# Optimization experiments

Measured on AMD Instinct MI355X. Metric: run time of the kernel, lower is better.

## Reference

```python
import jax, jax.numpy as jnp
import numpy as np
import math
from jax import lax

DIM = 96
D_MODEL = 2 * DIM            # SS2D d_model
D_INNER = 2 * D_MODEL        # expand = 2
D_STATE = 16
DT_RANK = math.ceil(D_MODEL / 16)
K = 4
B_, H_, W_ = 2, 48, 48


def setup_inputs() -> dict:
    key = jax.random.key(0)
    ks = jax.random.split(key, 12)
    r = lambda k, s, sc=0.02: jax.random.normal(k, s, jnp.float32) * sc
    A = np.tile(np.arange(1, D_STATE + 1, dtype=np.float32)[None, :], (K * D_INNER, 1))
    return dict(
        x=jax.random.normal(ks[0], (B_, DIM, H_, W_), jnp.float32),
        w_init=r(ks[1], (D_MODEL, DIM)),
        b_init=r(ks[2], (D_MODEL,)),
        w_fina=r(ks[3], (DIM, D_MODEL)),
        b_fina=r(ks[4], (DIM,)),
        in_proj_w=r(ks[5], (2 * D_INNER, D_MODEL)),
        conv_w=r(ks[6], (D_INNER, 1, 3, 3), 0.1),
        conv_b=r(ks[7], (D_INNER,)),
        x_proj_w=r(ks[8], (K, DT_RANK + 2 * D_STATE, D_INNER)),
        dt_w=r(ks[9], (K, D_INNER, DT_RANK), 0.1),
        dt_b=r(ks[10], (K, D_INNER), 0.1),
        A_logs=jnp.asarray(np.log(A)),
        Ds=jnp.ones((K * D_INNER,), jnp.float32),
        ln_g=jnp.ones((D_INNER,), jnp.float32),
        ln_b=jnp.zeros((D_INNER,), jnp.float32),
        out_proj_w=r(ks[11], (D_MODEL, D_INNER)),
    )


def _gelu(x):
    return jax.nn.gelu(x, approximate=False)


def _conv1x1(x, w, b):
    # x: (b,c,h,w), w: (o,c)
    return jnp.einsum('oc,bchw->bohw', w, x) + b[None, :, None, None]


def _ss2d(x, in_proj_w, conv_w, conv_b, x_proj_w, dt_w, dt_b, A_logs, Ds, ln_g, ln_b, out_proj_w):
    # x: (b, h, w, d_model)
    b, h, w, _ = x.shape
    L = h * w
    xz = jnp.einsum('bhwc,oc->bhwo', x, in_proj_w)          # (b,h,w,2*d_inner)
    xx, z = jnp.split(xz, 2, axis=-1)
    xc = xx.transpose(0, 3, 1, 2)                            # (b, d_inner, h, w)
    xc = lax.conv_general_dilated(xc, conv_w, (1, 1), 'SAME',
                                  feature_group_count=D_INNER,
                                  dimension_numbers=('NCHW', 'OIHW', 'NCHW'))
    xc = jax.nn.silu(xc + conv_b[None, :, None, None])
    # 4 scan directions: hw, wh, reversed hw, reversed wh
    x_hw = xc.reshape(b, D_INNER, L)
    x_wh = xc.transpose(0, 1, 3, 2).reshape(b, D_INNER, L)
    xs = jnp.stack([x_hw, x_wh, x_hw[..., ::-1], x_wh[..., ::-1]], axis=1)   # (b,K,d,L)
    x_dbl = jnp.einsum('bkdl,kcd->bkcl', xs, x_proj_w)
    dts = x_dbl[:, :, :DT_RANK]                               # (b,K,r,L)
    Bs = x_dbl[:, :, DT_RANK:DT_RANK + D_STATE]               # (b,K,n,L)
    Cs = x_dbl[:, :, DT_RANK + D_STATE:]                      # (b,K,n,L)
    dts = jnp.einsum('bkrl,kdr->bkdl', dts, dt_w)
    delta = jax.nn.softplus(dts + dt_b[None, :, :, None])     # (b,K,d,L)
    A = -jnp.exp(A_logs).reshape(K, D_INNER, D_STATE)         # (K,d,n)
    Dm = Ds.reshape(K, D_INNER)
    # selective scan over L (time-major stacked inputs)
    u_t = xs.transpose(3, 0, 1, 2)      # (L,b,K,d)
    dt_t = delta.transpose(3, 0, 1, 2)  # (L,b,K,d)
    B_t = Bs.transpose(3, 0, 1, 2)      # (L,b,K,n)
    C_t = Cs.transpose(3, 0, 1, 2)      # (L,b,K,n)
    h0 = jnp.zeros((b, K, D_INNER, D_STATE), xs.dtype)

    def step(hst, inp):
        u, dt, Bv, Cv = inp
        dA = jnp.exp(dt[..., None] * A)                       # (b,K,d,n)
        hst = dA * hst + (dt * u)[..., None] * Bv[:, :, None, :]
        y = jnp.einsum('bkdn,bkn->bkd', hst, Cv)
        return hst, y

    _, ys = lax.scan(step, h0, (u_t, dt_t, B_t, C_t))         # (L,b,K,d)
    ys = ys.transpose(1, 2, 3, 0) + Dm[None, :, :, None] * xs  # (b,K,d,L)
    y1 = ys[:, 0]
    y3 = ys[:, 2][..., ::-1]
    y2 = ys[:, 1].reshape(b, D_INNER, w, h).transpose(0, 1, 3, 2).reshape(b, D_INNER, L)
    y4 = ys[:, 3][..., ::-1].reshape(b, D_INNER, w, h).transpose(0, 1, 3, 2).reshape(b, D_INNER, L)
    y = (y1 + y2 + y3 + y4).transpose(0, 2, 1).reshape(b, h, w, D_INNER)
    mu = y.mean(-1, keepdims=True)
    var = y.var(-1, keepdims=True)
    y = (y - mu) / jnp.sqrt(var + 1e-5) * ln_g + ln_b
    y = y * jax.nn.silu(z)
    return jnp.einsum('bhwd,od->bhwo', y, out_proj_w)         # (b,h,w,d_model)


def _forward(x, w_init, b_init, w_fina, b_fina, in_proj_w, conv_w, conv_b,
             x_proj_w, dt_w, dt_b, A_logs, Ds, ln_g, ln_b, out_proj_w):
    x1 = _gelu(_conv1x1(x, w_init, b_init))                   # (b,2*dim,h,w)
    x0 = x1
    xt = x1.transpose(0, 2, 3, 1)                             # b h w c
    y = _ss2d(xt, in_proj_w, conv_w, conv_b, x_proj_w, dt_w, dt_b,
              A_logs, Ds, ln_g, ln_b, out_proj_w)
    y = y.transpose(0, 3, 1, 2)
    return _gelu(_conv1x1(y + x0, w_fina, b_fina))            # (b,dim,h,w)


def reference(x, w_init, b_init, w_fina, b_fina, in_proj_w, conv_w, conv_b,
              x_proj_w, dt_w, dt_b, A_logs, Ds, ln_g, ln_b, out_proj_w):
    return _forward(x, w_init, b_init, w_fina, b_fina, in_proj_w, conv_w, conv_b,
                    x_proj_w, dt_w, dt_b, A_logs, Ds, ln_g, ln_b, out_proj_w)
```

## Files before the change

kernel.cpp:

```cpp
#include <hip/hip_runtime.h>
#include <math.h>

#define LL 2304
#define HH 48
#define WW 48
#define BB 2
#define CI 96
#define DM 192
#define DI 384
#define KK 4
#define RR 12
#define NN 16
#define KC 44
#define CH 96
#define LEN 24

__device__ __forceinline__ float gelu_f(float x){
    return 0.5f*x*(1.0f+erff(x*0.70710678118654752f));
}
__device__ __forceinline__ float silu_f(float x){
    return x/(1.0f+__expf(-x));
}
__device__ __forceinline__ float softplus_f(float x){
    return fmaxf(x,0.0f) + log1pf(__expf(-fabsf(x)));
}

template<int C, int OT>
__device__ __forceinline__ void gemmN_acc(const float* __restrict__ xb, const float* __restrict__ w,
        int o0, float* wl, float acc[OT], int tid){
    for(int idx=tid; idx<OT*C; idx+=256) wl[idx] = w[(size_t)o0*C + idx];
    __syncthreads();
    #pragma unroll 2
    for(int c=0;c<C;c+=4){
        float x0=xb[(size_t)(c+0)*LL], x1=xb[(size_t)(c+1)*LL];
        float x2=xb[(size_t)(c+2)*LL], x3=xb[(size_t)(c+3)*LL];
        #pragma unroll
        for(int o=0;o<OT;o++){
            float4 wq = *reinterpret_cast<const float4*>(wl + o*C + c);
            acc[o] = fmaf(wq.x,x0, fmaf(wq.y,x1, fmaf(wq.z,x2, fmaf(wq.w,x3, acc[o]))));
        }
    }
}

__global__ __launch_bounds__(256) void k_init(const float* __restrict__ x, const float* __restrict__ w,
        const float* __restrict__ bias, float* __restrict__ x1){
    __shared__ float wl[8*CI];
    int l = blockIdx.x*256 + threadIdx.x;
    int o0 = blockIdx.y*8; int b = blockIdx.z;
    float acc[8];
    #pragma unroll
    for(int j=0;j<8;j++) acc[j] = bias[o0+j];
    gemmN_acc<CI,8>(x + (size_t)b*CI*LL + l, w, o0, wl, acc, threadIdx.x);
    float* ob = x1 + (size_t)b*DM*LL + o0*LL + l;
    #pragma unroll
    for(int j=0;j<8;j++) ob[j*LL] = gelu_f(acc[j]);
}

__global__ __launch_bounds__(256) void k_inproj(const float* __restrict__ x1, const float* __restrict__ w,
        float* __restrict__ xx, float* __restrict__ z){
    __shared__ float wl[16*DM];
    int l = blockIdx.x*256 + threadIdx.x;
    int o0 = blockIdx.y*16; int b = blockIdx.z;
    float acc[16];
    #pragma unroll
    for(int j=0;j<16;j++) acc[j] = 0.f;
    gemmN_acc<DM,16>(x1 + (size_t)b*DM*LL + l, w, o0, wl, acc, threadIdx.x);
    float* ob = (o0 < DI) ? (xx + (size_t)b*DI*LL + o0*LL + l)
                          : (z  + (size_t)b*DI*LL + (o0-DI)*LL + l);
    #pragma unroll
    for(int j=0;j<16;j++) ob[j*LL] = acc[j];
}

__global__ __launch_bounds__(256) void k_dwconv(const float* __restrict__ xx, const float* __restrict__ cw,
        const float* __restrict__ cb, float* __restrict__ xc){
    int l = blockIdx.x*256 + threadIdx.x;
    int d = blockIdx.y; int b = blockIdx.z;
    int h = l/WW, w = l%WW;
    const float* src = xx + ((size_t)b*DI + d)*LL;
    float acc = cb[d];
    #pragma unroll
    for(int dh=-1;dh<=1;dh++){
        int hh = h+dh; if(hh<0||hh>=HH) continue;
        #pragma unroll
        for(int dw=-1;dw<=1;dw++){
            int w2 = w+dw; if(w2<0||w2>=WW) continue;
            acc += cw[d*9 + (dh+1)*3 + (dw+1)] * src[hh*WW + w2];
        }
    }
    xc[((size_t)b*DI + d)*LL + l] = silu_f(acc);
}

__global__ __launch_bounds__(256) void k_proj(const float* __restrict__ xc, const float* __restrict__ w,
        float* __restrict__ pj){
    __shared__ float wl[8*DI];
    int l = blockIdx.x*256 + threadIdx.x;
    int o0 = blockIdx.y*8; int b = blockIdx.z;
    float acc[8];
    #pragma unroll
    for(int j=0;j<8;j++) acc[j] = 0.f;
    gemmN_acc<DI,8>(xc + (size_t)b*DI*LL + l, w, o0, wl, acc, threadIdx.x);
    float* ob = pj + ((size_t)b*(KK*KC) + o0)*LL + l;
    #pragma unroll
    for(int j=0;j<8;j++) ob[j*LL] = acc[j];
}

__global__ __launch_bounds__(256) void k_transpose(const float* __restrict__ xc, const float* __restrict__ z,
        float* __restrict__ xcT, float* __restrict__ zT){
    __shared__ float tile[32][33];
    int which = blockIdx.z >> 1;
    int b = blockIdx.z & 1;
    const float* src = which ? z : xc;
    float* dst = which ? zT : xcT;
    int l0 = blockIdx.x*32, d0 = blockIdx.y*32;
    int tx = threadIdx.x & 31, ty = threadIdx.x >> 5;
    #pragma unroll
    for(int j=0;j<4;j++)
        tile[ty+8*j][tx] = src[((size_t)b*DI + d0+ty+8*j)*LL + l0+tx];
    __syncthreads();
    #pragma unroll
    for(int j=0;j<4;j++)
        dst[((size_t)b*LL + l0+ty+8*j)*DI + d0+tx] = tile[tx][ty+8*j];
}

__global__ __launch_bounds__(256) void k_delta(const float* __restrict__ pj, const float* __restrict__ dtw,
        const float* __restrict__ dtb, float* __restrict__ deltaT){
    __shared__ float pjs[RR*32];
    int p0 = blockIdx.x*32;
    int bk = blockIdx.z; int b = bk>>2, k = bk&3;
    int lane = threadIdx.x & 63, sub = threadIdx.x >> 6;
    int d = blockIdx.y*64 + lane;
    const float* pjb = pj + ((size_t)b*(KK*KC) + k*KC)*LL;
    for(int idx=threadIdx.x; idx<RR*32; idx+=256){
        int r = idx>>5, pp = idx&31;
        pjs[idx] = pjb[(size_t)r*LL + p0+pp];
    }
    __syncthreads();
    float wr[RR];
    #pragma unroll
    for(int r=0;r<RR;r++) wr[r] = dtw[((size_t)k*DI + d)*RR + r];
    float dtbv = dtb[k*DI + d];
    #pragma unroll
    for(int i=0;i<8;i++){
        int pp = sub*8+i;
        float acc = dtbv;
        #pragma unroll
        for(int r=0;r<RR;r++) acc += wr[r]*pjs[r*32+pp];
        deltaT[((size_t)bk*LL + p0+pp)*DI + d] = softplus_f(acc);
    }
}

__device__ __forceinline__ int perm_pos(int k, int l){
    int lk = (k>=2) ? (LL-1-l) : l;
    return (k&1) ? ((lk%WW)*WW + lk/WW) : lk;
}

__global__ __launch_bounds__(384) void k_scan1(const float* __restrict__ xcT, const float* __restrict__ pj,
        const float* __restrict__ deltaT, const float* __restrict__ alogs,
        float* __restrict__ gbuf, float* __restrict__ Sbuf){
    __shared__ float bs[LEN*16];
    int chunk = blockIdx.x;
    int bk = blockIdx.y; int b = bk>>2, k = bk&3;
    int lane = threadIdx.x & 63, wv = threadIdx.x >> 6;
    int d = wv*64 + lane;
    const float* pjb = pj + ((size_t)b*(KK*KC) + k*KC)*LL;
    for(int idx=threadIdx.x; idx<LEN*16; idx+=384){
        int s = idx>>4, n = idx&15;
        int p = perm_pos(k, chunk*LEN+s);
        bs[idx] = pjb[(size_t)(RR+n)*LL + p];
    }
    __syncthreads();
    float a[NN], h[NN];
    #pragma unroll
    for(int n=0;n<NN;n++){ a[n] = -__expf(alogs[((size_t)k*DI + d)*NN + n]); h[n]=0.f; }
    float S = 0.f;
    const float* dptr = deltaT + (size_t)bk*LL*DI + d;
    const float* uptr = xcT + (size_t)b*LL*DI + d;
    for(int s=0;s<LEN;s++){
        int p = perm_pos(k, chunk*LEN+s);
        float dt = dptr[(size_t)p*DI];
        float u  = uptr[(size_t)p*DI];
        S += dt;
        float du = dt*u;
        #pragma unroll
        for(int nq=0;nq<4;nq++){
            float4 Bq = *reinterpret_cast<const float4*>(bs + s*16 + nq*4);
            h[nq*4+0] = __expf(dt*a[nq*4+0])*h[nq*4+0] + du*Bq.x;
            h[nq*4+1] = __expf(dt*a[nq*4+1])*h[nq*4+1] + du*Bq.y;
            h[nq*4+2] = __expf(dt*a[nq*4+2])*h[nq*4+2] + du*Bq.z;
            h[nq*4+3] = __expf(dt*a[nq*4+3])*h[nq*4+3] + du*Bq.w;
        }
    }
    int base = (bk*CH + chunk)*NN;
    #pragma unroll
    for(int n=0;n<NN;n++) gbuf[(size_t)(base+n)*DI + d] = h[n];
    Sbuf[(size_t)(bk*CH + chunk)*DI + d] = S;
}

__global__ __launch_bounds__(256) void k_scan2(const float* __restrict__ alogs, const float* __restrict__ Sbuf,
        float* __restrict__ gbuf){
    int id = blockIdx.x*256 + threadIdx.x;
    int d = id % DI;
    int n = (id/DI) % NN;
    int bk = id/(DI*NN);
    int k = bk & 3;
    float a = -__expf(alogs[((size_t)k*DI + d)*NN + n]);
    float h = 0.f;
    for(int j=0;j<CH;j++){
        float S = Sbuf[(size_t)(bk*CH + j)*DI + d];
        size_t gi = (size_t)((bk*CH + j)*NN + n)*DI + d;
        float g = gbuf[gi];
        gbuf[gi] = h;
        h = __expf(a*S)*h + g;
    }
}

__global__ __launch_bounds__(384) void k_scan3(const float* __restrict__ xcT, const float* __restrict__ pj,
        const float* deltaT, const float* __restrict__ alogs,
        const float* __restrict__ gbuf, float* yout){
    __shared__ float bs[LEN*32];
    int chunk = blockIdx.x;
    int bk = blockIdx.y; int b = bk>>2, k = bk&3;
    int lane = threadIdx.x & 63, wv = threadIdx.x >> 6;
    int d = wv*64 + lane;
    const float* pjb = pj + ((size_t)b*(KK*KC) + k*KC)*LL;
    for(int idx=threadIdx.x; idx<LEN*32; idx+=384){
        int s = idx>>5, c = idx&31;
        int p = perm_pos(k, chunk*LEN+s);
        bs[idx] = pjb[(size_t)(RR+c)*LL + p];
    }
    __syncthreads();
    float a[NN], h[NN];
    int base = (bk*CH + chunk)*NN;
    #pragma unroll
    for(int n=0;n<NN;n++){
        a[n] = -__expf(alogs[((size_t)k*DI + d)*NN + n]);
        h[n] = gbuf[(size_t)(base+n)*DI + d];
    }
    const float* dptr = deltaT + (size_t)bk*LL*DI + d;
    const float* uptr = xcT + (size_t)b*LL*DI + d;
    float* yptr = yout + (size_t)bk*LL*DI + d;
    for(int s=0;s<LEN;s++){
        int p = perm_pos(k, chunk*LEN+s);
        float dt = dptr[(size_t)p*DI];
        float u  = uptr[(size_t)p*DI];
        float du = dt*u;
        float y = 0.f;
        #pragma unroll
        for(int nq=0;nq<4;nq++){
            float4 Bq = *reinterpret_cast<const float4*>(bs + s*32 + nq*4);
            float4 Cq = *reinterpret_cast<const float4*>(bs + s*32 + 16 + nq*4);
            h[nq*4+0] = __expf(dt*a[nq*4+0])*h[nq*4+0] + du*Bq.x;  y += h[nq*4+0]*Cq.x;
            h[nq*4+1] = __expf(dt*a[nq*4+1])*h[nq*4+1] + du*Bq.y;  y += h[nq*4+1]*Cq.y;
            h[nq*4+2] = __expf(dt*a[nq*4+2])*h[nq*4+2] + du*Bq.z;  y += h[nq*4+2]*Cq.z;
            h[nq*4+3] = __expf(dt*a[nq*4+3])*h[nq*4+3] + du*Bq.w;  y += h[nq*4+3]*Cq.w;
        }
        yptr[(size_t)p*DI] = y;
    }
}

__global__ __launch_bounds__(256) void k_merge(const float* __restrict__ yout, const float* __restrict__ xcT,
        const float* __restrict__ zT, const float* __restrict__ Ds,
        const float* __restrict__ lng, const float* __restrict__ lnb,
        float* __restrict__ ygT){
    __shared__ float tile[32*385];
    int p0 = blockIdx.x*32; int b = blockIdx.y;
    for(int idx=threadIdx.x; idx<32*DI; idx+=256){
        int pp = idx/DI, d = idx%DI; int p = p0+pp;
        float dsum = Ds[d] + Ds[DI+d] + Ds[2*DI+d] + Ds[3*DI+d];
        float v = dsum * xcT[((size_t)b*LL + p)*DI + d];
        #pragma unroll
        for(int kk=0;kk<4;kk++) v += yout[((size_t)(b*4+kk)*LL + p)*DI + d];
        tile[pp*385 + d] = v;
    }
    __syncthreads();
    int lane = threadIdx.x & 63, wv = threadIdx.x >> 6;
    for(int i=0;i<8;i++){
        int pp = wv*8 + i; int p = p0+pp;
        float s1=0.f, s2=0.f;
        float vals[6];
        #pragma unroll
        for(int j=0;j<6;j++){ float v = tile[pp*385 + lane + 64*j]; vals[j]=v; s1+=v; s2+=v*v; }
        #pragma unroll
        for(int m=1;m<64;m<<=1){ s1 += __shfl_xor(s1,m); s2 += __shfl_xor(s2,m); }
        float mu = s1*(1.0f/DI);
        float var = s2*(1.0f/DI) - mu*mu;
        float rstd = rsqrtf(var + 1e-5f);
        #pragma unroll
        for(int j=0;j<6;j++){
            int c = lane + 64*j;
            float zv = zT[((size_t)b*LL + p)*DI + c];
            float y = (vals[j]-mu)*rstd*lng[c] + lnb[c];
            tile[pp*385 + c] = y * silu_f(zv);
        }
    }
    __syncthreads();
    for(int idx=threadIdx.x; idx<32*DI; idx+=256){
        int pp = idx & 31, d = idx >> 5;
        ygT[((size_t)b*DI + d)*LL + p0 + pp] = tile[pp*385 + d];
    }
}

__global__ __launch_bounds__(256) void k_outproj(const float* __restrict__ ygT, const float* __restrict__ w,
        const float* __restrict__ x1, float* __restrict__ yo){
    __shared__ float wl[8*DI];
    int l = blockIdx.x*256 + threadIdx.x;
    int o0 = blockIdx.y*8; int b = blockIdx.z;
    float acc[8];
    #pragma unroll
    for(int j=0;j<8;j++) acc[j] = 0.f;
    gemmN_acc<DI,8>(ygT + (size_t)b*DI*LL + l, w, o0, wl, acc, threadIdx.x);
    const float* rb = x1 + (size_t)b*DM*LL + o0*LL + l;
    float* ob = yo + (size_t)b*DM*LL + o0*LL + l;
    #pragma unroll
    for(int j=0;j<8;j++) ob[j*LL] = acc[j] + rb[j*LL];
}

__global__ __launch_bounds__(256) void k_final(const float* __restrict__ yo,
        const float* __restrict__ w, const float* __restrict__ bias, float* __restrict__ out){
    __shared__ float wl[4*DM];
    int l = blockIdx.x*256 + threadIdx.x;
    int o0 = blockIdx.y*4; int b = blockIdx.z;
    float acc[4];
    #pragma unroll
    for(int j=0;j<4;j++) acc[j] = bias[o0+j];
    gemmN_acc<DM,4>(yo + (size_t)b*DM*LL + l, w, o0, wl, acc, threadIdx.x);
    float* ob = out + (size_t)b*CI*LL + o0*LL + l;
    #pragma unroll
    for(int j=0;j<4;j++) ob[j*LL] = gelu_f(acc[j]);
}

extern "C" void kernel_launch(void* const* d_in, const int* in_sizes, int n_in,
                              void* d_out, int out_size, void* d_ws, size_t ws_size,
                              hipStream_t stream) {
    const float* x        = (const float*)d_in[0];
    const float* w_init   = (const float*)d_in[1];
    const float* b_init   = (const float*)d_in[2];
    const float* w_fina   = (const float*)d_in[3];
    const float* b_fina   = (const float*)d_in[4];
    const float* in_proj_w= (const float*)d_in[5];
    const float* conv_w   = (const float*)d_in[6];
    const float* conv_b   = (const float*)d_in[7];
    const float* x_proj_w = (const float*)d_in[8];
    const float* dt_w     = (const float*)d_in[9];
    const float* dt_b     = (const float*)d_in[10];
    const float* A_logs   = (const float*)d_in[11];
    const float* Ds       = (const float*)d_in[12];
    const float* ln_g     = (const float*)d_in[13];
    const float* ln_b     = (const float*)d_in[14];
    const float* out_proj_w=(const float*)d_in[15];

    float* ws = (float*)d_ws;
    float* x1   = ws;
    float* xx   = x1 + 884736;
    float* z    = xx + 1769472;
    float* xc   = z  + 1769472;
    float* xcT  = xc + 1769472;
    float* zT   = xcT+ 1769472;
    float* pj   = zT + 1769472;
    float* deltaT = pj + 811008;

    float* gbuf = xx;
    float* Sbuf = xx + 4718592;
    float* yout = deltaT;
    float* ygT  = xx;
    float* yo   = z;

    dim3 blk(256);
    k_init   <<<dim3(9,24,BB), blk, 0, stream>>>(x, w_init, b_init, x1);
    k_inproj <<<dim3(9,48,BB), blk, 0, stream>>>(x1, in_proj_w, xx, z);
    k_dwconv <<<dim3(9,DI,BB), blk, 0, stream>>>(xx, conv_w, conv_b, xc);
    k_proj   <<<dim3(9,22,BB), blk, 0, stream>>>(xc, x_proj_w, pj);
    k_transpose<<<dim3(72,12,2*BB), blk, 0, stream>>>(xc, z, xcT, zT);
    k_delta  <<<dim3(72,6,BB*KK), blk, 0, stream>>>(pj, dt_w, dt_b, deltaT);
    k_scan1  <<<dim3(CH,BB*KK), dim3(384), 0, stream>>>(xcT, pj, deltaT, A_logs, gbuf, Sbuf);
    k_scan2  <<<dim3(192), blk, 0, stream>>>(A_logs, Sbuf, gbuf);
    k_scan3  <<<dim3(CH,BB*KK), dim3(384), 0, stream>>>(xcT, pj, deltaT, A_logs, gbuf, yout);
    k_merge  <<<dim3(72,BB), blk, 0, stream>>>(yout, xcT, zT, Ds, ln_g, ln_b, ygT);
    k_outproj<<<dim3(9,24,BB), blk, 0, stream>>>(ygT, out_proj_w, x1, yo);
    k_final  <<<dim3(9,24,BB), blk, 0, stream>>>(yo, w_fina, b_fina, (float*)d_out);
}
```

Before: 360.7 us.

## Move in/x/out projection GEMMs to split-bf16 MFMA with transposed activations

Replaces the scalar FP32 GEMMs for in_proj, x_proj and out_proj with MFMA 16x16x32 bf16 kernels. Each operand is split into high and low bf16 parts, and three products are summed to keep near-FP32 accuracy. Producer kernels (init, transpose, merge) now also emit token-major bf16 hi/lo copies, and a new kernel converts the weights on every call. The aim is to cut ALU-bound GEMM time. In exchange it adds extra buffer writes, per-call weight conversion, and direct global loads without LDS staging, and it drops the low*low term.

```diff
diff --git a/kernel.cpp b/kernel.cpp
--- a/kernel.cpp
+++ b/kernel.cpp
@@ -15,6 +15,9 @@
 #define CH 96
 #define LEN 24
 
+typedef short bf16x8 __attribute__((ext_vector_type(8)));
+typedef float f32x4 __attribute__((ext_vector_type(4)));
+
 __device__ __forceinline__ float gelu_f(float x){
     return 0.5f*x*(1.0f+erff(x*0.70710678118654752f));
 }
@@ -23,6 +26,16 @@
 }
 __device__ __forceinline__ float softplus_f(float x){
     return fmaxf(x,0.0f) + log1pf(__expf(-fabsf(x)));
+}
+__device__ __forceinline__ unsigned short bf16_rne(float x){
+    unsigned u = __float_as_uint(x);
+    unsigned r = (u + 0x7FFFu + ((u>>16)&1u)) >> 16;
+    return (unsigned short)r;
+}
+__device__ __forceinline__ void split_bf16(float x, unsigned short& h, unsigned short& l){
+    h = bf16_rne(x);
+    float fh = __uint_as_float(((unsigned)h)<<16);
+    l = bf16_rne(x - fh);
 }
 
 template<int C, int OT>
@@ -42,8 +55,56 @@
     }
 }
 
+__global__ __launch_bounds__(256) void k_convw(const float* __restrict__ ipw, const float* __restrict__ xpw,
+        const float* __restrict__ opw, short* __restrict__ wh_ip, short* __restrict__ wl_ip,
+        short* __restrict__ wh_xp, short* __restrict__ wl_xp,
+        short* __restrict__ wh_op, short* __restrict__ wl_op){
+    int idx = blockIdx.x*256 + threadIdx.x;
+    unsigned short h, l;
+    if(idx < 147456){
+        split_bf16(ipw[idx], h, l); wh_ip[idx]=h; wl_ip[idx]=l;
+    } else if(idx < 147456+67584){
+        int j = idx - 147456;
+        split_bf16(xpw[j], h, l); wh_xp[j]=h; wl_xp[j]=l;
+    } else {
+        int j = idx - 215040;
+        split_bf16(opw[j], h, l); wh_op[j]=h; wl_op[j]=l;
+    }
+}
+
+template<int K>
+__device__ __forceinline__ void mfma_core(const short* __restrict__ Ah, const short* __restrict__ Al,
+        const short* __restrict__ Bh, const short* __restrict__ Bl, f32x4 acc[2][4]){
+    int lane = threadIdx.x & 63;
+    int rl = lane & 15, g = lane >> 4;
+    #pragma unroll
+    for(int kc=0; kc<K; kc+=32){
+        bf16x8 ah[2], al[2], bh[4], bl[4];
+        #pragma unroll
+        for(int mi=0;mi<2;mi++){
+            ah[mi] = *reinterpret_cast<const bf16x8*>(Ah + (size_t)(mi*16+rl)*K + kc + g*8);
+            al[mi] = *reinterpret_cast<const bf16x8*>(Al + (size_t)(mi*16+rl)*K + kc + g*8);
+        }
+        #pragma unroll
+        for(int ni=0;ni<4;ni++){
+            bh[ni] = *reinterpret_cast<const bf16x8*>(Bh + (size_t)(ni*16+rl)*K + kc + g*8);
+            bl[ni] = *reinterpret_cast<const bf16x8*>(Bl + (size_t)(ni*16+rl)*K + kc + g*8);
+        }
+        #pragma unroll
+        for(int mi=0;mi<2;mi++){
+            #pragma unroll
+            for(int ni=0;ni<4;ni++){
+                acc[mi][ni] = __builtin_amdgcn_mfma_f32_16x16x32_bf16(ah[mi], bh[ni], acc[mi][ni], 0,0,0);
+                acc[mi][ni] = __builtin_amdgcn_mfma_f32_16x16x32_bf16(ah[mi], bl[ni], acc[mi][ni], 0,0,0);
+                acc[mi][ni] = __builtin_amdgcn_mfma_f32_16x16x32_bf16(al[mi], bh[ni], acc[mi][ni], 0,0,0);
+            }
+        }
+    }
+}
+
 __global__ __launch_bounds__(256) void k_init(const float* __restrict__ x, const float* __restrict__ w,
-        const float* __restrict__ bias, float* __restrict__ x1){
+        const float* __restrict__ bias, float* __restrict__ x1,
+        short* __restrict__ x1Th, short* __restrict__ x1Tl){
     __shared__ float wl[8*CI];
     int l = blockIdx.x*256 + threadIdx.x;
     int o0 = blockIdx.y*8; int b = blockIdx.z;
@@ -52,23 +113,51 @@
     for(int j=0;j<8;j++) acc[j] = bias[o0+j];
     gemmN_acc<CI,8>(x + (size_t)b*CI*LL + l, w, o0, wl, acc, threadIdx.x);
     float* ob = x1 + (size_t)b*DM*LL + o0*LL + l;
-    #pragma unroll
-    for(int j=0;j<8;j++) ob[j*LL] = gelu_f(acc[j]);
-}
-
-__global__ __launch_bounds__(256) void k_inproj(const float* __restrict__ x1, const float* __restrict__ w,
+    unsigned hw[4], lw[4];
+    #pragma unroll
+    for(int j=0;j<8;j+=2){
+        float g0 = gelu_f(acc[j]), g1 = gelu_f(acc[j+1]);
+        ob[j*LL] = g0; ob[(j+1)*LL] = g1;
+        unsigned short h0,l0,h1,l1;
+        split_bf16(g0,h0,l0); split_bf16(g1,h1,l1);
+        hw[j>>1] = (unsigned)h0 | ((unsigned)h1<<16);
+        lw[j>>1] = (unsigned)l0 | ((unsigned)l1<<16);
+    }
+    size_t tbase = ((size_t)b*LL + l)*DM + o0;
+    *reinterpret_cast<uint4*>(x1Th + tbase) = make_uint4(hw[0],hw[1],hw[2],hw[3]);
+    *reinterpret_cast<uint4*>(x1Tl + tbase) = make_uint4(lw[0],lw[1],lw[2],lw[3]);
+}
+
+__global__ __launch_bounds__(256) void k_inproj(const short* __restrict__ wh, const short* __restrict__ wlo,
+        const short* __restrict__ x1Th, const short* __restrict__ x1Tl,
         float* __restrict__ xx, float* __restrict__ z){
-    __shared__ float wl[16*DM];
-    int l = blockIdx.x*256 + threadIdx.x;
-    int o0 = blockIdx.y*16; int b = blockIdx.z;
-    float acc[16];
-    #pragma unroll
-    for(int j=0;j<16;j++) acc[j] = 0.f;
-    gemmN_acc<DM,16>(x1 + (size_t)b*DM*LL + l, w, o0, wl, acc, threadIdx.x);
-    float* ob = (o0 < DI) ? (xx + (size_t)b*DI*LL + o0*LL + l)
-                          : (z  + (size_t)b*DI*LL + (o0-DI)*LL + l);
-    #pragma unroll
-    for(int j=0;j<16;j++) ob[j*LL] = acc[j];
+    int w = threadIdx.x >> 6, lane = threadIdx.x & 63;
+    int wm = w >> 1, wn = w & 1;
+    int m0 = blockIdx.y*64 + wm*32;
+    int n0 = blockIdx.x*128 + wn*64;
+    int b = blockIdx.z;
+    f32x4 acc[2][4];
+    #pragma unroll
+    for(int mi=0;mi<2;mi++)
+        #pragma unroll
+        for(int ni=0;ni<4;ni++) acc[mi][ni] = (f32x4){0.f,0.f,0.f,0.f};
+    mfma_core<DM>(wh + (size_t)m0*DM, wlo + (size_t)m0*DM,
+                  x1Th + ((size_t)b*LL + n0)*DM, x1Tl + ((size_t)b*LL + n0)*DM, acc);
+    int rl = lane & 15, g = lane >> 4;
+    #pragma unroll
+    for(int mi=0;mi<2;mi++){
+        #pragma unroll
+        for(int ni=0;ni<4;ni++){
+            #pragma unroll
+            for(int i=0;i<4;i++){
+                int m = m0 + mi*16 + g*4 + i;
+                int l = n0 + ni*16 + rl;
+                float v = acc[mi][ni][i];
+                if(m < DI) xx[((size_t)b*DI + m)*LL + l] = v;
+                else       z [((size_t)b*DI + (m-DI))*LL + l] = v;
+            }
+        }
+    }
 }
 
 __global__ __launch_bounds__(256) void k_dwconv(const float* __restrict__ xx, const float* __restrict__ cw,
@@ -90,22 +179,9 @@
     xc[((size_t)b*DI + d)*LL + l] = silu_f(acc);
 }
 
-__global__ __launch_bounds__(256) void k_proj(const float* __restrict__ xc, const float* __restrict__ w,
-        float* __restrict__ pj){
-    __shared__ float wl[8*DI];
-    int l = blockIdx.x*256 + threadIdx.x;
-    int o0 = blockIdx.y*8; int b = blockIdx.z;
-    float acc[8];
-    #pragma unroll
-    for(int j=0;j<8;j++) acc[j] = 0.f;
-    gemmN_acc<DI,8>(xc + (size_t)b*DI*LL + l, w, o0, wl, acc, threadIdx.x);
-    float* ob = pj + ((size_t)b*(KK*KC) + o0)*LL + l;
-    #pragma unroll
-    for(int j=0;j<8;j++) ob[j*LL] = acc[j];
-}
-
 __global__ __launch_bounds__(256) void k_transpose(const float* __restrict__ xc, const float* __restrict__ z,
-        float* __restrict__ xcT, float* __restrict__ zT){
+        float* __restrict__ xcT, float* __restrict__ zT,
+        short* __restrict__ xcTh, short* __restrict__ xcTl){
     __shared__ float tile[32][33];
     int which = blockIdx.z >> 1;
     int b = blockIdx.z & 1;
@@ -118,8 +194,47 @@
         tile[ty+8*j][tx] = src[((size_t)b*DI + d0+ty+8*j)*LL + l0+tx];
     __syncthreads();
     #pragma unroll
-    for(int j=0;j<4;j++)
-        dst[((size_t)b*LL + l0+ty+8*j)*DI + d0+tx] = tile[tx][ty+8*j];
+    for(int j=0;j<4;j++){
+        float v = tile[tx][ty+8*j];
+        size_t di = ((size_t)b*LL + l0+ty+8*j)*DI + d0+tx;
+        dst[di] = v;
+        if(!which){
+            unsigned short h,l;
+            split_bf16(v,h,l);
+            xcTh[di] = (short)h; xcTl[di] = (short)l;
+        }
+    }
+}
+
+__global__ __launch_bounds__(256) void k_proj(const short* __restrict__ wh, const short* __restrict__ wlo,
+        const short* __restrict__ xcTh, const short* __restrict__ xcTl,
+        float* __restrict__ pj){
+    int w = threadIdx.x >> 6, lane = threadIdx.x & 63;
+    int wm = w >> 1, wn = w & 1;
+    int m0 = blockIdx.y*64 + wm*32;
+    int n0 = blockIdx.x*128 + wn*64;
+    int b = blockIdx.z;
+    f32x4 acc[2][4];
+    #pragma unroll
+    for(int mi=0;mi<2;mi++)
+        #pragma unroll
+        for(int ni=0;ni<4;ni++) acc[mi][ni] = (f32x4){0.f,0.f,0.f,0.f};
+    mfma_core<DI>(wh + (size_t)m0*DI, wlo + (size_t)m0*DI,
+                  xcTh + ((size_t)b*LL + n0)*DI, xcTl + ((size_t)b*LL + n0)*DI, acc);
+    int rl = lane & 15, g = lane >> 4;
+    #pragma unroll
+    for(int mi=0;mi<2;mi++){
+        #pragma unroll
+        for(int ni=0;ni<4;ni++){
+            #pragma unroll
+            for(int i=0;i<4;i++){
+                int m = m0 + mi*16 + g*4 + i;
+                if(m >= KK*KC) continue;
+                int l = n0 + ni*16 + rl;
+                pj[((size_t)b*(KK*KC) + m)*LL + l] = acc[mi][ni][i];
+            }
+        }
+    }
 }
 
 __global__ __launch_bounds__(256) void k_delta(const float* __restrict__ pj, const float* __restrict__ dtw,
@@ -261,7 +376,7 @@
 __global__ __launch_bounds__(256) void k_merge(const float* __restrict__ yout, const float* __restrict__ xcT,
         const float* __restrict__ zT, const float* __restrict__ Ds,
         const float* __restrict__ lng, const float* __restrict__ lnb,
-        float* __restrict__ ygT){
+        short* __restrict__ ygh, short* __restrict__ ygl){
     __shared__ float tile[32*385];
     int p0 = blockIdx.x*32; int b = blockIdx.y;
     for(int idx=threadIdx.x; idx<32*DI; idx+=256){
@@ -290,29 +405,44 @@
             int c = lane + 64*j;
             float zv = zT[((size_t)b*LL + p)*DI + c];
             float y = (vals[j]-mu)*rstd*lng[c] + lnb[c];
-            tile[pp*385 + c] = y * silu_f(zv);
-        }
-    }
-    __syncthreads();
-    for(int idx=threadIdx.x; idx<32*DI; idx+=256){
-        int pp = idx & 31, d = idx >> 5;
-        ygT[((size_t)b*DI + d)*LL + p0 + pp] = tile[pp*385 + d];
-    }
-}
-
-__global__ __launch_bounds__(256) void k_outproj(const float* __restrict__ ygT, const float* __restrict__ w,
+            float gv = y * silu_f(zv);
+            unsigned short h,l;
+            split_bf16(gv,h,l);
+            size_t oi = ((size_t)b*LL + p)*DI + c;
+            ygh[oi] = (short)h; ygl[oi] = (short)l;
+        }
+    }
+}
+
+__global__ __launch_bounds__(256) void k_outproj(const short* __restrict__ wh, const short* __restrict__ wlo,
+        const short* __restrict__ ygh, const short* __restrict__ ygl,
         const float* __restrict__ x1, float* __restrict__ yo){
-    __shared__ float wl[8*DI];
-    int l = blockIdx.x*256 + threadIdx.x;
-    int o0 = blockIdx.y*8; int b = blockIdx.z;
-    float acc[8];
-    #pragma unroll
-    for(int j=0;j<8;j++) acc[j] = 0.f;
-    gemmN_acc<DI,8>(ygT + (size_t)b*DI*LL + l, w, o0, wl, acc, threadIdx.x);
-    const float* rb = x1 + (size_t)b*DM*LL + o0*LL + l;
-    float* ob = yo + (size_t)b*DM*LL + o0*LL + l;
-    #pragma unroll
-    for(int j=0;j<8;j++) ob[j*LL] = acc[j] + rb[j*LL];
+    int w = threadIdx.x >> 6, lane = threadIdx.x & 63;
+    int wm = w >> 1, wn = w & 1;
+    int m0 = blockIdx.y*64 + wm*32;
+    int n0 = blockIdx.x*128 + wn*64;
+    int b = blockIdx.z;
+    f32x4 acc[2][4];
+    #pragma unroll
+    for(int mi=0;mi<2;mi++)
+        #pragma unroll
+        for(int ni=0;ni<4;ni++) acc[mi][ni] = (f32x4){0.f,0.f,0.f,0.f};
+    mfma_core<DI>(wh + (size_t)m0*DI, wlo + (size_t)m0*DI,
+                  ygh + ((size_t)b*LL + n0)*DI, ygl + ((size_t)b*LL + n0)*DI, acc);
+    int rl = lane & 15, g = lane >> 4;
+    #pragma unroll
+    for(int mi=0;mi<2;mi++){
+        #pragma unroll
+        for(int ni=0;ni<4;ni++){
+            #pragma unroll
+            for(int i=0;i<4;i++){
+                int m = m0 + mi*16 + g*4 + i;
+                int l = n0 + ni*16 + rl;
+                size_t oi = ((size_t)b*DM + m)*LL + l;
+                yo[oi] = acc[mi][ni][i] + x1[oi];
+            }
+        }
+    }
 }
 
 __global__ __launch_bounds__(256) void k_final(const float* __restrict__ yo,
@@ -358,24 +488,40 @@
     float* zT   = xcT+ 1769472;
     float* pj   = zT + 1769472;
     float* deltaT = pj + 811008;
+    float* wcvt = deltaT + 7077888;
+
+    short* wh_ip = (short*)wcvt;
+    short* wl_ip = wh_ip + 147456;
+    short* wh_xp = wl_ip + 147456;
+    short* wl_xp = wh_xp + 73728;
+    short* wh_op = wl_xp + 73728;
+    short* wl_op = wh_op + 73728;
+
+    short* x1Th = (short*)deltaT;
+    short* x1Tl = x1Th + 884736;
+    short* xcTh = x1Tl + 884736;
+    short* xcTl = xcTh + 1769472;
 
     float* gbuf = xx;
     float* Sbuf = xx + 4718592;
     float* yout = deltaT;
-    float* ygT  = xx;
+    short* ygh  = (short*)xc;
+    short* ygl  = ygh + 1769472;
     float* yo   = z;
 
     dim3 blk(256);
-    k_init   <<<dim3(9,24,BB), blk, 0, stream>>>(x, w_init, b_init, x1);
-    k_inproj <<<dim3(9,48,BB), blk, 0, stream>>>(x1, in_proj_w, xx, z);
+    k_convw  <<<dim3(1128), blk, 0, stream>>>(in_proj_w, x_proj_w, out_proj_w,
+                                              wh_ip, wl_ip, wh_xp, wl_xp, wh_op, wl_op);
+    k_init   <<<dim3(9,24,BB), blk, 0, stream>>>(x, w_init, b_init, x1, x1Th, x1Tl);
+    k_inproj <<<dim3(18,12,BB), blk, 0, stream>>>(wh_ip, wl_ip, x1Th, x1Tl, xx, z);
     k_dwconv <<<dim3(9,DI,BB), blk, 0, stream>>>(xx, conv_w, conv_b, xc);
-    k_proj   <<<dim3(9,22,BB), blk, 0, stream>>>(xc, x_proj_w, pj);
-    k_transpose<<<dim3(72,12,2*BB), blk, 0, stream>>>(xc, z, xcT, zT);
+    k_transpose<<<dim3(72,12,2*BB), blk, 0, stream>>>(xc, z, xcT, zT, xcTh, xcTl);
+    k_proj   <<<dim3(18,3,BB), blk, 0, stream>>>(wh_xp, wl_xp, xcTh, xcTl, pj);
     k_delta  <<<dim3(72,6,BB*KK), blk, 0, stream>>>(pj, dt_w, dt_b, deltaT);
     k_scan1  <<<dim3(CH,BB*KK), dim3(384), 0, stream>>>(xcT, pj, deltaT, A_logs, gbuf, Sbuf);
     k_scan2  <<<dim3(192), blk, 0, stream>>>(A_logs, Sbuf, gbuf);
     k_scan3  <<<dim3(CH,BB*KK), dim3(384), 0, stream>>>(xcT, pj, deltaT, A_logs, gbuf, yout);
-    k_merge  <<<dim3(72,BB), blk, 0, stream>>>(yout, xcT, zT, Ds, ln_g, ln_b, ygT);
-    k_outproj<<<dim3(9,24,BB), blk, 0, stream>>>(ygT, out_proj_w, x1, yo);
+    k_merge  <<<dim3(72,BB), blk, 0, stream>>>(yout, xcT, zT, Ds, ln_g, ln_b, ygh, ygl);
+    k_outproj<<<dim3(18,3,BB), blk, 0, stream>>>(wh_op, wl_op, ygh, ygl, x1, yo);
     k_final  <<<dim3(9,24,BB), blk, 0, stream>>>(yo, w_fina, b_fina, (float*)d_out);
 }
```

Result: faster. 325.1 us (-9.9%).
